# Optimization experiments

Measured on AMD Instinct MI355X. Metric: run time of the kernel, lower is better.

The kernel has to match this reference:

```python
import jax, jax.numpy as jnp
import numpy as np

B, H, N, D = 4, 8, 2048, 64  # d_model=512, n_heads=8 -> d_head=64
MASK_PROB = 0.1
SCALE = D ** -0.5


def setup_inputs() -> dict:
    key = jax.random.key(0)
    kq, kk, kv, km = jax.random.split(key, 4)
    q = jax.random.normal(kq, (B, H, N, D), dtype=jnp.float32)
    k = jax.random.normal(kk, (B, H, N, D), dtype=jnp.float32)
    v = jax.random.normal(kv, (B, H, N, D), dtype=jnp.float32)
    # torch.bernoulli(full(..., prob)): 1 with prob=mask_prob -> dropped
    mask = jax.random.bernoulli(km, MASK_PROB, (B, H, N, N))
    return {"q": q, "k": k, "v": v, "mask": mask}


def reference(q, k, v, mask):
    # [B,H,N,N] scores: QK^T * scale -> tanh -> zero where mask is True
    scores = jnp.tanh(jnp.einsum("bhnd,bhmd->bhnm", q, k) * SCALE)
    scores = scores * (~mask).astype(scores.dtype)
    return jnp.einsum("bhnm,bhmd->bhnd", scores, v)
```

## Files before the change

### kernel.cpp

```cpp
#include <hip/hip_runtime.h>
#include <hip/hip_bf16.h>

namespace {

constexpr int N = 2048;
constexpr int D = 64;
constexpr float SCALE = 0.125f;
constexpr int LSTR = 72;
constexpr int NT = N / 64;

typedef __attribute__((ext_vector_type(8))) short bf16x8;
typedef __attribute__((ext_vector_type(4))) float f32x4;
typedef __attribute__((ext_vector_type(4))) short short4v;

__device__ inline short f2bf(float x) {
  union { float f; unsigned u; } a; a.f = x;
  unsigned r = a.u + 0x7fffu + ((a.u >> 16) & 1u);
  return (short)(r >> 16);
}

__device__ inline float fast_tanh(float x) {
  float e = __builtin_amdgcn_exp2f(x * 2.885390081777927f);
  return 1.0f - 2.0f * __builtin_amdgcn_rcpf(e + 1.0f);
}

}

__global__ __launch_bounds__(256) void attn_tanh_kernel(
    const float* __restrict__ Q, const float* __restrict__ K,
    const float* __restrict__ V, const int* __restrict__ M,
    float* __restrict__ O)
{
  __shared__ __align__(16) short k_s[64 * LSTR];
  __shared__ __align__(16) short vt_s[64 * LSTR];
  __shared__ __align__(16) short s_s[64 * LSTR];

  const int tid  = threadIdx.x;
  const int wave = tid >> 6;
  const int lane = tid & 63;
  const int l15  = lane & 15;
  const int quad = lane >> 4;

  const int bh = blockIdx.x >> 5;
  const int q0 = (blockIdx.x & 31) * 64;

  const float* qp = Q + (size_t)bh * N * D;
  const float* kp = K + (size_t)bh * N * D;
  const float* vp = V + (size_t)bh * N * D;
  const int*   mp = M + (size_t)bh * N * N;
  float* op = O + (size_t)bh * N * D;

  bf16x8 qf[2];
  {
    const float* qrow = qp + (size_t)(q0 + wave * 16 + l15) * D + quad * 8;
#pragma unroll
    for (int ks = 0; ks < 2; ++ks) {
      float4 f0 = *(const float4*)(qrow + ks * 32);
      float4 f1 = *(const float4*)(qrow + ks * 32 + 4);
      bf16x8 t;
      t[0] = f2bf(f0.x); t[1] = f2bf(f0.y); t[2] = f2bf(f0.z); t[3] = f2bf(f0.w);
      t[4] = f2bf(f1.x); t[5] = f2bf(f1.y); t[6] = f2bf(f1.z); t[7] = f2bf(f1.w);
      qf[ks] = t;
    }
  }

  const int r0 = tid >> 4;
  const int c4 = (tid & 15) << 2;

  float4 kreg[4], vreg[4];
  int mreg[16];
  const int* mbase = mp + (size_t)(q0 + wave * 16 + quad * 4) * N + l15;

#pragma unroll
  for (int i = 0; i < 4; ++i) {
    kreg[i] = *(const float4*)(kp + (size_t)(i * 16 + r0) * D + c4);
    vreg[i] = *(const float4*)(vp + (size_t)(i * 16 + r0) * D + c4);
  }
#pragma unroll
  for (int r = 0; r < 4; ++r)
#pragma unroll
    for (int ct = 0; ct < 4; ++ct)
      mreg[r * 4 + ct] = __builtin_nontemporal_load(mbase + (size_t)r * N + ct * 16);

  f32x4 o_acc[4];
#pragma unroll
  for (int i = 0; i < 4; ++i) o_acc[i] = (f32x4){0.f, 0.f, 0.f, 0.f};

  for (int kt = 0; kt < NT; ++kt) {
    __syncthreads();

#pragma unroll
    for (int i = 0; i < 4; ++i) {
      int row = i * 16 + r0;
      short4v kv;
      kv[0] = f2bf(kreg[i].x); kv[1] = f2bf(kreg[i].y);
      kv[2] = f2bf(kreg[i].z); kv[3] = f2bf(kreg[i].w);
      *(short4v*)(&k_s[row * LSTR + c4]) = kv;
      vt_s[(c4 + 0) * LSTR + row] = f2bf(vreg[i].x);
      vt_s[(c4 + 1) * LSTR + row] = f2bf(vreg[i].y);
      vt_s[(c4 + 2) * LSTR + row] = f2bf(vreg[i].z);
      vt_s[(c4 + 3) * LSTR + row] = f2bf(vreg[i].w);
    }
    __syncthreads();

#pragma unroll
    for (int ct = 0; ct < 4; ++ct) {
      f32x4 acc = {0.f, 0.f, 0.f, 0.f};
#pragma unroll
      for (int ks = 0; ks < 2; ++ks) {
        bf16x8 b = *(const bf16x8*)(&k_s[(ct * 16 + l15) * LSTR + quad * 8 + ks * 32]);
        acc = __builtin_amdgcn_mfma_f32_16x16x32_bf16(qf[ks], b, acc, 0, 0, 0);
      }
#pragma unroll
      for (int r = 0; r < 4; ++r) {
        float s = fast_tanh(acc[r] * SCALE);
        s = mreg[r * 4 + ct] ? 0.0f : s;
        s_s[(wave * 16 + quad * 4 + r) * LSTR + ct * 16 + l15] = f2bf(s);
      }
    }

    if (kt + 1 < NT) {
      const float* kpt = kp + (size_t)(kt + 1) * 64 * D;
      const float* vpt = vp + (size_t)(kt + 1) * 64 * D;
#pragma unroll
      for (int i = 0; i < 4; ++i) {
        kreg[i] = *(const float4*)(kpt + (size_t)(i * 16 + r0) * D + c4);
        vreg[i] = *(const float4*)(vpt + (size_t)(i * 16 + r0) * D + c4);
      }
      const int* mb = mbase + (size_t)(kt + 1) * 64;
#pragma unroll
      for (int r = 0; r < 4; ++r)
#pragma unroll
        for (int ct = 0; ct < 4; ++ct)
          mreg[r * 4 + ct] = __builtin_nontemporal_load(mb + (size_t)r * N + ct * 16);
    }

    const short* srow = &s_s[(wave * 16 + l15) * LSTR + quad * 8];
#pragma unroll
    for (int ks = 0; ks < 2; ++ks) {
      bf16x8 a = *(const bf16x8*)(srow + ks * 32);
#pragma unroll
      for (int nt = 0; nt < 4; ++nt) {
        bf16x8 b = *(const bf16x8*)(&vt_s[(nt * 16 + l15) * LSTR + quad * 8 + ks * 32]);
        o_acc[nt] = __builtin_amdgcn_mfma_f32_16x16x32_bf16(a, b, o_acc[nt], 0, 0, 0);
      }
    }
  }

#pragma unroll
  for (int nt = 0; nt < 4; ++nt) {
#pragma unroll
    for (int r = 0; r < 4; ++r) {
      op[(q0 + wave * 16 + quad * 4 + r) * D + nt * 16 + l15] = o_acc[nt][r];
    }
  }
}

extern "C" void kernel_launch(void* const* d_in, const int* in_sizes, int n_in,
                              void* d_out, int out_size, void* d_ws, size_t ws_size,
                              hipStream_t stream) {
  const float* q = (const float*)d_in[0];
  const float* k = (const float*)d_in[1];
  const float* v = (const float*)d_in[2];
  const int* m = (const int*)d_in[3];
  float* out = (float*)d_out;

  attn_tanh_kernel<<<dim3(1024), dim3(256), 0, stream>>>(q, k, v, m, out);
}
```

Measured before the change: 759.3 us.

## Transpose QK MFMA output and vectorize mask, V-transpose and score stores

Swaps the MFMA operand order so each lane holds four consecutive key columns of a score row. The mask can then be read as one 16-byte int4 load per column tile instead of scalar loads, and scores are written to shared memory as 4-short vector stores. V is now loaded column-wise per lane so its transpose into shared memory uses vector stores, with a padded stride of 68 to reduce bank conflicts. The trade-off is that V loads become 16 scalar strided loads per thread, and the B-fragment reads become two 8-byte LDS reads.

```diff
diff --git a/kernel.cpp b/kernel.cpp
--- a/kernel.cpp
+++ b/kernel.cpp
@@ -1,17 +1,18 @@
 #include <hip/hip_runtime.h>
-#include <hip/hip_bf16.h>
 
 namespace {
 
 constexpr int N = 2048;
 constexpr int D = 64;
 constexpr float SCALE = 0.125f;
-constexpr int LSTR = 72;
+constexpr int LK = 72;
+constexpr int LV = 68;
 constexpr int NT = N / 64;
 
 typedef __attribute__((ext_vector_type(8))) short bf16x8;
+typedef __attribute__((ext_vector_type(4))) short short4v;
 typedef __attribute__((ext_vector_type(4))) float f32x4;
-typedef __attribute__((ext_vector_type(4))) short short4v;
+typedef __attribute__((ext_vector_type(4))) int   int4v;
 
 __device__ inline short f2bf(float x) {
   union { float f; unsigned u; } a; a.f = x;
@@ -31,9 +32,9 @@
     const float* __restrict__ V, const int* __restrict__ M,
     float* __restrict__ O)
 {
-  __shared__ __align__(16) short k_s[64 * LSTR];
-  __shared__ __align__(16) short vt_s[64 * LSTR];
-  __shared__ __align__(16) short s_s[64 * LSTR];
+  __shared__ __align__(16) short k_s[64 * LK];
+  __shared__ __align__(16) short s_s[64 * LK];
+  __shared__ __align__(16) short vt_s[64 * LV];
 
   const int tid  = threadIdx.x;
   const int wave = tid >> 6;
@@ -67,20 +68,22 @@
   const int r0 = tid >> 4;
   const int c4 = (tid & 15) << 2;
 
-  float4 kreg[4], vreg[4];
-  int mreg[16];
-  const int* mbase = mp + (size_t)(q0 + wave * 16 + quad * 4) * N + l15;
+  float4 kreg[4];
+  float  vreg[16];
+  int4v  mreg[4];
+
+  const float* vbase = vp + (size_t)(wave * 16) * D + lane;
+  const int*   mbase = mp + (size_t)(q0 + wave * 16 + l15) * N + quad * 4;
 
 #pragma unroll
-  for (int i = 0; i < 4; ++i) {
+  for (int i = 0; i < 4; ++i)
     kreg[i] = *(const float4*)(kp + (size_t)(i * 16 + r0) * D + c4);
-    vreg[i] = *(const float4*)(vp + (size_t)(i * 16 + r0) * D + c4);
-  }
 #pragma unroll
-  for (int r = 0; r < 4; ++r)
+  for (int i = 0; i < 16; ++i)
+    vreg[i] = vbase[(size_t)i * D];
 #pragma unroll
-    for (int ct = 0; ct < 4; ++ct)
-      mreg[r * 4 + ct] = __builtin_nontemporal_load(mbase + (size_t)r * N + ct * 16);
+  for (int ct = 0; ct < 4; ++ct)
+    mreg[ct] = __builtin_nontemporal_load((const int4v*)(mbase + ct * 16));
 
   f32x4 o_acc[4];
 #pragma unroll
@@ -91,15 +94,17 @@
 
 #pragma unroll
     for (int i = 0; i < 4; ++i) {
-      int row = i * 16 + r0;
       short4v kv;
       kv[0] = f2bf(kreg[i].x); kv[1] = f2bf(kreg[i].y);
       kv[2] = f2bf(kreg[i].z); kv[3] = f2bf(kreg[i].w);
-      *(short4v*)(&k_s[row * LSTR + c4]) = kv;
-      vt_s[(c4 + 0) * LSTR + row] = f2bf(vreg[i].x);
-      vt_s[(c4 + 1) * LSTR + row] = f2bf(vreg[i].y);
-      vt_s[(c4 + 2) * LSTR + row] = f2bf(vreg[i].z);
-      vt_s[(c4 + 3) * LSTR + row] = f2bf(vreg[i].w);
+      *(short4v*)(&k_s[(i * 16 + r0) * LK + c4]) = kv;
+    }
+#pragma unroll
+    for (int c = 0; c < 4; ++c) {
+      short4v vv;
+      vv[0] = f2bf(vreg[4 * c + 0]); vv[1] = f2bf(vreg[4 * c + 1]);
+      vv[2] = f2bf(vreg[4 * c + 2]); vv[3] = f2bf(vreg[4 * c + 3]);
+      *(short4v*)(&vt_s[lane * LV + wave * 16 + 4 * c]) = vv;
     }
     __syncthreads();
 
@@ -108,40 +113,42 @@
       f32x4 acc = {0.f, 0.f, 0.f, 0.f};
 #pragma unroll
       for (int ks = 0; ks < 2; ++ks) {
-        bf16x8 b = *(const bf16x8*)(&k_s[(ct * 16 + l15) * LSTR + quad * 8 + ks * 32]);
-        acc = __builtin_amdgcn_mfma_f32_16x16x32_bf16(qf[ks], b, acc, 0, 0, 0);
+        bf16x8 a = *(const bf16x8*)(&k_s[(ct * 16 + l15) * LK + ks * 32 + quad * 8]);
+        acc = __builtin_amdgcn_mfma_f32_16x16x32_bf16(a, qf[ks], acc, 0, 0, 0);
       }
+      short4v sv;
 #pragma unroll
       for (int r = 0; r < 4; ++r) {
         float s = fast_tanh(acc[r] * SCALE);
-        s = mreg[r * 4 + ct] ? 0.0f : s;
-        s_s[(wave * 16 + quad * 4 + r) * LSTR + ct * 16 + l15] = f2bf(s);
+        sv[r] = mreg[ct][r] ? (short)0 : f2bf(s);
       }
+      *(short4v*)(&s_s[(wave * 16 + l15) * LK + ct * 16 + quad * 4]) = sv;
     }
 
     if (kt + 1 < NT) {
       const float* kpt = kp + (size_t)(kt + 1) * 64 * D;
-      const float* vpt = vp + (size_t)(kt + 1) * 64 * D;
 #pragma unroll
-      for (int i = 0; i < 4; ++i) {
+      for (int i = 0; i < 4; ++i)
         kreg[i] = *(const float4*)(kpt + (size_t)(i * 16 + r0) * D + c4);
-        vreg[i] = *(const float4*)(vpt + (size_t)(i * 16 + r0) * D + c4);
-      }
+      const float* vpt = vbase + (size_t)(kt + 1) * 64 * D;
+#pragma unroll
+      for (int i = 0; i < 16; ++i)
+        vreg[i] = vpt[(size_t)i * D];
       const int* mb = mbase + (size_t)(kt + 1) * 64;
 #pragma unroll
-      for (int r = 0; r < 4; ++r)
-#pragma unroll
-        for (int ct = 0; ct < 4; ++ct)
-          mreg[r * 4 + ct] = __builtin_nontemporal_load(mb + (size_t)r * N + ct * 16);
+      for (int ct = 0; ct < 4; ++ct)
+        mreg[ct] = __builtin_nontemporal_load((const int4v*)(mb + ct * 16));
     }
 
-    const short* srow = &s_s[(wave * 16 + l15) * LSTR + quad * 8];
 #pragma unroll
     for (int ks = 0; ks < 2; ++ks) {
-      bf16x8 a = *(const bf16x8*)(srow + ks * 32);
+      bf16x8 a = *(const bf16x8*)(&s_s[(wave * 16 + l15) * LK + ks * 32 + quad * 8]);
 #pragma unroll
       for (int nt = 0; nt < 4; ++nt) {
-        bf16x8 b = *(const bf16x8*)(&vt_s[(nt * 16 + l15) * LSTR + quad * 8 + ks * 32]);
+        const short* vb = &vt_s[(nt * 16 + l15) * LV + ks * 32 + quad * 8];
+        short4v lo = *(const short4v*)(vb);
+        short4v hi = *(const short4v*)(vb + 4);
+        bf16x8 b = __builtin_shufflevector(lo, hi, 0, 1, 2, 3, 4, 5, 6, 7);
         o_acc[nt] = __builtin_amdgcn_mfma_f32_16x16x32_bf16(a, b, o_acc[nt], 0, 0, 0);
       }
     }
```

Result: no change. 758.5 us (-0.1%).
